# Optimization experiments

Measured on AMD Instinct MI355X. Metric: run time of the kernel, lower is better.

Reference implementation:

```python
import jax, jax.numpy as jnp
import numpy as np

B, L, D, H, DH, DFF, NL, A = 32, 1024, 512, 8, 64, 2048, 6, 21
CL = 4  # new variables per clique (chain junction tree)


def _build_mask():
    # Mirrors _make_junction_tree_mask: each position attends to itself,
    # to all parent-clique variables, and to earlier vars in its own clique.
    m = np.zeros((L, L), dtype=bool)
    for c in range(L // CL):
        own = range(c * CL, (c + 1) * CL)
        par = range((c - 1) * CL, c * CL) if c > 0 else range(0)
        for i in own:
            m[i, i] = True
            for p in par:
                m[i, p] = True
            for v in own:
                if v < i:
                    m[i, v] = True
    return m


def setup_inputs() -> dict:
    key = jax.random.key(0)
    ks = jax.random.split(key, 12)
    s = 0.02
    inp = {
        "x": jax.random.randint(ks[0], (B, L), 0, A, dtype=jnp.int32),
        "mask": jnp.asarray(_build_mask())[None, None],  # (1,1,L,L), broadcasts over B,H
        "tok_emb": jax.random.normal(ks[1], (A, D)) * s,
        "pos_emb": jax.random.normal(ks[2], (L, D)) * s,
        "wq": jax.random.normal(ks[3], (NL, D, D)) * s,
        "bq": jnp.zeros((NL, D)),
        "wk": jax.random.normal(ks[4], (NL, D, D)) * s,
        "bk": jnp.zeros((NL, D)),
        "wv": jax.random.normal(ks[5], (NL, D, D)) * s,
        "bv": jnp.zeros((NL, D)),
        "wo": jax.random.normal(ks[6], (NL, D, D)) * s,
        "bo": jnp.zeros((NL, D)),
        "ln1_s": jnp.ones((NL, D)),
        "ln1_b": jnp.zeros((NL, D)),
        "ln2_s": jnp.ones((NL, D)),
        "ln2_b": jnp.zeros((NL, D)),
        "w1": jax.random.normal(ks[7], (NL, D, DFF)) * s,
        "b1": jnp.zeros((NL, DFF)),
        "w2": jax.random.normal(ks[8], (NL, DFF, D)) * s,
        "b2": jnp.zeros((NL, D)),
        "wout": jax.random.normal(ks[9], (D, A)) * s,
        "bout": jnp.zeros((A,)),
    }
    return inp


def _ln(x, s, b):
    mu = x.mean(-1, keepdims=True)
    var = ((x - mu) ** 2).mean(-1, keepdims=True)
    return (x - mu) * jax.lax.rsqrt(var + 1e-6) * s + b


def reference(x, mask, tok_emb, pos_emb, wq, bq, wk, bk, wv, bv, wo, bo,
              ln1_s, ln1_b, ln2_s, ln2_b, w1, b1, w2, b2, wout, bout):
    h = tok_emb[x] + pos_emb[None, :, :]           # (B, L, D)
    neg = jnp.asarray(-1e9, h.dtype)
    scale = jnp.asarray(1.0 / np.sqrt(DH), h.dtype)
    for l in range(NL):
        # masked multi-head self-attention (pre-LN block)
        hn = _ln(h, ln1_s[l], ln1_b[l])
        q = (hn @ wq[l] + bq[l]).reshape(B, L, H, DH)
        k = (hn @ wk[l] + bk[l]).reshape(B, L, H, DH)
        v = (hn @ wv[l] + bv[l]).reshape(B, L, H, DH)
        sc = jnp.einsum('blhd,bmhd->bhlm', q, k) * scale
        sc = jnp.where(mask, sc, neg)              # junction-tree sparsity pattern
        attn = jax.nn.softmax(sc, axis=-1)
        o = jnp.einsum('bhlm,bmhd->blhd', attn, v).reshape(B, L, D) @ wo[l] + bo[l]
        h = h + o
        # feed-forward
        hn = _ln(h, ln2_s[l], ln2_b[l])
        h = h + (jax.nn.gelu(hn @ w1[l] + b1[l]) @ w2[l] + b2[l])
    return h @ wout + bout                          # (B, L, alphabet_size)
```

## Files before the change

### kernel.cpp

```cpp
#include <hip/hip_runtime.h>

#define BB 32
#define LL 1024
#define DD 512
#define HH 8
#define DHH 64
#define DFF 2048
#define NLAYERS 6
#define AA 21
#define MTOT (BB*LL)
#define QS 1536

typedef unsigned short u16;
typedef __bf16 bf16x8 __attribute__((ext_vector_type(8)));
typedef float f32x4 __attribute__((ext_vector_type(4)));
typedef u16 u16x8 __attribute__((ext_vector_type(8)));

__device__ __forceinline__ float bf2f(u16 u) {
    return __uint_as_float(((unsigned int)u) << 16);
}
__device__ __forceinline__ u16 f2bf(float f) {
    unsigned int i = __float_as_uint(f);
    unsigned int r = i + 0x7FFFu + ((i >> 16) & 1u);
    return (u16)(r >> 16);
}

__global__ void detect_kernel(const void* __restrict__ tok, int* __restrict__ flag) {
    __shared__ int cnt[256];
    int t = threadIdx.x;
    const u16* p = (const u16*)tok;
    int c = 0;
    #pragma unroll
    for (int j = 0; j < 8; j++) {
        u16 u = p[2 * (t * 8 + j)];
        int e = (u >> 7) & 0xFF;
        c += (e >= 97 && e <= 137) ? 1 : 0;
    }
    cnt[t] = c;
    __syncthreads();
    for (int s = 128; s; s >>= 1) {
        if (t < s) cnt[t] += cnt[t + s];
        __syncthreads();
    }
    if (t == 0) flag[0] = (cnt[0] > 1024) ? 1 : 0;
}

#define NTAB 13
struct ConvTab {
    const void* src[NTAB];
    unsigned long long dstOff[NTAB];
    int n[NTAB];
    int chunk[NTAB];
    int lstride[NTAB];
};
__global__ __launch_bounds__(256) void conv_small(ConvTab tab, u16* __restrict__ spBase,
                                                  const int* __restrict__ flag, int total) {
    int i = blockIdx.x * 256 + threadIdx.x;
    if (i >= total) return;
    int fl = flag[0];
    #pragma unroll 1
    for (int e = 0; e < NTAB; e++) {
        if (i < tab.n[e]) {
            const void* s = tab.src[e];
            u16 val = fl ? ((const u16*)s)[i] : f2bf(((const float*)s)[i]);
            int c = i / tab.chunk[e];
            int r = i - c * tab.chunk[e];
            spBase[tab.dstOff[e] + (size_t)c * tab.lstride[e] + r] = val;
            return;
        }
        i -= tab.n[e];
    }
}

__global__ __launch_bounds__(256) void conv_T(const void* __restrict__ src,
                                              u16* __restrict__ dst, int R, int C,
                                              const int* __restrict__ flag, int dstZS) {
    __shared__ u16 tile[32][33];
    int z = blockIdx.z;
    size_t zoffS = (size_t)z * R * C;
    size_t zoffD = (size_t)z * dstZS;
    int bx = blockIdx.x * 32, by = blockIdx.y * 32;
    int tx = threadIdx.x & 31, ty = threadIdx.x >> 5;
    int fl = flag[0];
    const u16* s16 = (const u16*)src + zoffS;
    const float* s32 = (const float*)src + zoffS;
    #pragma unroll
    for (int r = 0; r < 4; r++) {
        size_t idx = (size_t)(by + ty * 4 + r) * C + bx + tx;
        tile[ty * 4 + r][tx] = fl ? s16[idx] : f2bf(s32[idx]);
    }
    __syncthreads();
    #pragma unroll
    for (int r = 0; r < 4; r++)
        dst[zoffD + (size_t)(bx + ty * 4 + r) * R + by + tx] = tile[tx][ty * 4 + r];
}

__global__ __launch_bounds__(256) void woutpad_kernel(const void* __restrict__ wout,
                                                      const void* __restrict__ bout,
                                                      u16* __restrict__ wpad,
                                                      u16* __restrict__ bpad,
                                                      const int* __restrict__ flag) {
    int i = blockIdx.x * 256 + threadIdx.x;
    int fl = flag[0];
    if (i < 128 * 512) {
        int n = i >> 9, kk = i & 511;
        u16 val = 0;
        if (n < AA) val = fl ? ((const u16*)wout)[kk * AA + n] : f2bf(((const float*)wout)[kk * AA + n]);
        wpad[(size_t)n * 512 + kk] = val;
    }
    if (i < 128) {
        u16 val = 0;
        if (i < AA) val = fl ? ((const u16*)bout)[i] : f2bf(((const float*)bout)[i]);
        bpad[i] = val;
    }
}

__global__ __launch_bounds__(128) void embed_kernel(const int* __restrict__ x,
                                                    const u16* __restrict__ tok_emb,
                                                    const u16* __restrict__ pos_emb,
                                                    float* __restrict__ h) {
    int row = blockIdx.x;
    int l = row & (LL - 1);
    int tok = x[row];
    int c = threadIdx.x * 4;
    ushort4 te = *(const ushort4*)(tok_emb + (size_t)tok * DD + c);
    ushort4 pe = *(const ushort4*)(pos_emb + (size_t)l * DD + c);
    float4 o;
    o.x = bf2f(te.x) + bf2f(pe.x);
    o.y = bf2f(te.y) + bf2f(pe.y);
    o.z = bf2f(te.z) + bf2f(pe.z);
    o.w = bf2f(te.w) + bf2f(pe.w);
    *(float4*)(h + (size_t)row * DD + c) = o;
}

__global__ __launch_bounds__(256) void ln_kernel(const float* __restrict__ h,
                                                 const u16* __restrict__ s,
                                                 const u16* __restrict__ b,
                                                 u16* __restrict__ outp) {
    int row = blockIdx.x * 4 + (threadIdx.x >> 6);
    int lane = threadIdx.x & 63;
    const float* hr = h + (size_t)row * DD + lane * 8;
    f32x4 v0 = *(const f32x4*)hr;
    f32x4 v1 = *(const f32x4*)(hr + 4);
    float sum = v0[0]+v0[1]+v0[2]+v0[3]+v1[0]+v1[1]+v1[2]+v1[3];
    #pragma unroll
    for (int off = 32; off; off >>= 1) sum += __shfl_xor(sum, off, 64);
    float mu = sum * (1.0f / DD);
    float var = 0.f;
    #pragma unroll
    for (int i = 0; i < 4; i++) {
        float d0 = v0[i] - mu, d1 = v1[i] - mu;
        var += d0 * d0 + d1 * d1;
    }
    #pragma unroll
    for (int off = 32; off; off >>= 1) var += __shfl_xor(var, off, 64);
    float rs = rsqrtf(var * (1.0f / DD) + 1e-6f);
    u16x8 sv = *(const u16x8*)(s + lane * 8);
    u16x8 bv = *(const u16x8*)(b + lane * 8);
    u16x8 o;
    #pragma unroll
    for (int i = 0; i < 8; i++) {
        float xv = (i < 4) ? v0[i] : v1[i - 4];
        o[i] = f2bf((xv - mu) * rs * bf2f(sv[i]) + bf2f(bv[i]));
    }
    *(u16x8*)(outp + (size_t)row * DD + lane * 8) = o;
}

#define GLD16(gp, lp) __builtin_amdgcn_global_load_lds( \
    (const __attribute__((address_space(1))) void*)(gp), \
    (__attribute__((address_space(3))) void*)(lp), 16, 0, 0)
#define WAIT_VM(n) asm volatile("s_waitcnt vmcnt(" #n ") lgkmcnt(0)" ::: "memory")

template <int EPI>
__global__ __launch_bounds__(256) void gemm_bt(const u16* __restrict__ A,
                                               const u16* __restrict__ BT,
                                               const u16* __restrict__ bias,
                                               u16* __restrict__ Cb,
                                               float* __restrict__ Cf,
                                               int M, int N, int K, int lda,
                                               const int* __restrict__ flag) {
    __shared__ __align__(16) u16 Als[3][128 * 32];
    __shared__ __align__(16) u16 Bls[3][128 * 32];
    const int tid  = threadIdx.x;
    const int lane = tid & 63;
    const int wave = tid >> 6;

    int gx = gridDim.x, gy = gridDim.y;
    int tileX, tileY;
    if ((gy & 7) == 0) {
        int bid = blockIdx.y * gx + blockIdx.x;
        int xcd = bid & 7;
        int idx = bid >> 3;
        int stripe = gy >> 3;
        tileX = idx % gx;
        tileY = xcd * stripe + idx / gx;
    } else {
        tileX = blockIdx.x; tileY = blockIdx.y;
    }
    const int tileM = tileY * 128;
    const int tileN = tileX * 128;
    const int wm = (wave & 1) * 64;
    const int wn = (wave >> 1) * 64;

    const int srow = tid >> 2;
    const int scol = (((tid & 3) ^ ((tid >> 3) & 3))) * 8;

    const u16* Ag0 = A  + (size_t)(tileM + srow) * lda + scol;
    const u16* Ag1 = A  + (size_t)(tileM + 64 + srow) * lda + scol;
    const u16* Bg0 = BT + (size_t)(tileN + srow) * K + scol;
    const u16* Bg1 = BT + (size_t)(tileN + 64 + srow) * K + scol;

    f32x4 acc[4][4] = {};
    const int lm = lane & 15;
    const int lk = (((lane >> 4) ^ ((lm >> 1) & 3))) * 8;

    const int nk = K >> 5;

    {
        GLD16(Ag0, Als[0] + tid * 8);
        GLD16(Ag1, Als[0] + 2048 + tid * 8);
        GLD16(Bg0, Bls[0] + tid * 8);
        GLD16(Bg1, Bls[0] + 2048 + tid * 8);
        GLD16(Ag0 + 32, Als[1] + tid * 8);
        GLD16(Ag1 + 32, Als[1] + 2048 + tid * 8);
        GLD16(Bg0 + 32, Bls[1] + tid * 8);
        GLD16(Bg1 + 32, Bls[1] + 2048 + tid * 8);
    }
    WAIT_VM(4);
    __builtin_amdgcn_s_barrier();

    int cur = 0;
    int stg = 2;
    for (int kt = 0; kt < nk; kt++) {
        if (kt + 2 < nk) {
            const int k2 = (kt + 2) << 5;
            GLD16(Ag0 + k2, Als[stg] + tid * 8);
            GLD16(Ag1 + k2, Als[stg] + 2048 + tid * 8);
            GLD16(Bg0 + k2, Bls[stg] + tid * 8);
            GLD16(Bg1 + k2, Bls[stg] + 2048 + tid * 8);
        }
        bf16x8 af[4], bfr[4];
        #pragma unroll
        for (int i = 0; i < 4; i++)
            af[i] = *(const bf16x8*)(Als[cur] + (wm + i * 16 + lm) * 32 + lk);
        #pragma unroll
        for (int j = 0; j < 4; j++)
            bfr[j] = *(const bf16x8*)(Bls[cur] + (wn + j * 16 + lm) * 32 + lk);
        #pragma unroll
        for (int i = 0; i < 4; i++)
            #pragma unroll
            for (int j = 0; j < 4; j++)
                acc[i][j] = __builtin_amdgcn_mfma_f32_16x16x32_bf16(af[i], bfr[j], acc[i][j], 0, 0, 0);
        if (kt + 1 < nk) {
            if (kt + 2 < nk) WAIT_VM(4);
            else             WAIT_VM(0);
            __builtin_amdgcn_s_barrier();
        }
        cur = (cur == 2) ? 0 : cur + 1;
        stg = (stg == 2) ? 0 : stg + 1;
    }

    int fl = 0;
    if constexpr (EPI == 3) fl = flag[0];
    const int r0 = (lane >> 4) * 4;
    #pragma unroll
    for (int j = 0; j < 4; j++) {
        int col = tileN + wn + j * 16 + lm;
        float bv = bf2f(bias[col]);
        #pragma unroll
        for (int i = 0; i < 4; i++) {
            int row = tileM + wm + i * 16 + r0;
            #pragma unroll
            for (int r = 0; r < 4; r++) {
                float xv = acc[i][j][r] + bv;
                if constexpr (EPI == 0) {
                    Cb[(size_t)(row + r) * N + col] = f2bf(xv);
                } else if constexpr (EPI == 1) {
                    float u = 1.5957691216057308f * (xv + 0.044715f * xv * xv * xv);
                    float t = 1.0f - 2.0f / (__expf(u) + 1.0f);
                    Cb[(size_t)(row + r) * N + col] = f2bf(0.5f * xv * (1.0f + t));
                } else if constexpr (EPI == 2) {
                    Cf[(size_t)(row + r) * N + col] += xv;
                } else if constexpr (EPI == 4) {
                    size_t idx = (size_t)(row + r) * N + col;
                    Cb[idx] = f2bf(xv + Cf[idx]);
                } else {
                    if (col < AA) {
                        size_t idx = (size_t)(row + r) * AA + col;
                        if (fl) Cb[idx] = f2bf(xv);
                        else    Cf[idx] = xv;
                    }
                }
            }
        }
    }
}

__global__ __launch_bounds__(256) void attn_kernel(u16* qkv) {
    int bl   = blockIdx.x * 4 + (threadIdx.x >> 6);
    int lane = threadIdx.x & 63;
    int l    = bl & (LL - 1);
    int lo   = (l & ~3) - 4; if (lo < 0) lo = 0;
    int nj   = l - lo + 1;

    size_t qrow = (size_t)bl * QS;
    int off = lane * 8;

    u16x8 q8 = *(const u16x8*)(qkv + qrow + off);
    float qf[8];
    #pragma unroll
    for (int i = 0; i < 8; i++) qf[i] = bf2f(q8[i]) * 0.125f;

    size_t base = (size_t)(bl - (l - lo)) * QS;
    float sc[8];
    u16x8 v8[8];
    #pragma unroll
    for (int j = 0; j < 8; j++) {
        int jc = (j < nj) ? j : (nj - 1);
        const u16* krow = qkv + base + (size_t)jc * QS;
        u16x8 k8 = *(const u16x8*)(krow + 512 + off);
        v8[j]    = *(const u16x8*)(krow + 1024 + off);
        float t = 0.f;
        #pragma unroll
        for (int i = 0; i < 8; i++) t = fmaf(qf[i], bf2f(k8[i]), t);
        t += __shfl_xor(t, 1, 64);
        t += __shfl_xor(t, 2, 64);
        t += __shfl_xor(t, 4, 64);
        sc[j] = (j < nj) ? t : -1e30f;
    }
    float m = sc[0];
    #pragma unroll
    for (int j = 1; j < 8; j++) m = fmaxf(m, sc[j]);
    float p[8], den = 0.f;
    #pragma unroll
    for (int j = 0; j < 8; j++) { p[j] = __expf(sc[j] - m); den += p[j]; }
    float inv = 1.0f / den;
    float o[8] = {};
    #pragma unroll
    for (int j = 0; j < 8; j++)
        #pragma unroll
        for (int i = 0; i < 8; i++) o[i] = fmaf(p[j], bf2f(v8[j][i]), o[i]);
    u16x8 ov;
    #pragma unroll
    for (int i = 0; i < 8; i++) ov[i] = f2bf(o[i] * inv);
    *(u16x8*)(qkv + qrow + off) = ov;
}

extern "C" void kernel_launch(void* const* d_in, const int* in_sizes, int n_in,
                              void* d_out, int out_size, void* d_ws, size_t ws_size,
                              hipStream_t stream) {
    const int base = n_in - 22;
    const int*  x    = (const int*)d_in[0];
    const void* tokI = d_in[2 + base];
    const void* posI = d_in[3 + base];
    const void* wqI  = d_in[4 + base];
    const void* bqI  = d_in[5 + base];
    const void* wkI  = d_in[6 + base];
    const void* bkI  = d_in[7 + base];
    const void* wvI  = d_in[8 + base];
    const void* bvI  = d_in[9 + base];
    const void* woI  = d_in[10 + base];
    const void* boI  = d_in[11 + base];
    const void* ln1sI = d_in[12 + base];
    const void* ln1bI = d_in[13 + base];
    const void* ln2sI = d_in[14 + base];
    const void* ln2bI = d_in[15 + base];
    const void* w1I  = d_in[16 + base];
    const void* b1I  = d_in[17 + base];
    const void* w2I  = d_in[18 + base];
    const void* b2I  = d_in[19 + base];
    const void* woutI = d_in[20 + base];
    const void* boutI = d_in[21 + base];

    char* ws = (char*)d_ws;
    float* h   = (float*)(ws + 0);
    u16*  hn   = (u16*)(ws + 67108864);
    u16*  qkv  = (u16*)(ws + 100663296);
    u16*  wT   = (u16*)(ws + 201326592);
    u16*  sp   = (u16*)(ws + 239075328);
    int* flag  = (int*)(ws + 240500736);

    u16* mid = qkv;

    u16* wqkvT = wT;
    u16* woT   = wT + 4718592;
    u16* w1T   = wT + 6291456;
    u16* w2T   = wT + 12582912;

    const unsigned long long oWoutPad = 0;
    const unsigned long long oBoutPad = 65536;
    const unsigned long long oTok     = 65664;
    const unsigned long long oPos     = 76416;
    const unsigned long long oQkvB    = 600704;
    const unsigned long long oBo      = 609920;
    const unsigned long long oB1      = 612992;
    const unsigned long long oB2      = 625280;
    const unsigned long long oLn1s    = 628352;
    const unsigned long long oLn1b    = 631424;
    const unsigned long long oLn2s    = 634496;
    const unsigned long long oLn2b    = 637568;

    detect_kernel<<<1, 256, 0, stream>>>(tokI, flag);

    ConvTab tab;
    const void* srcs[NTAB] = {tokI, bqI, bkI, bvI, boI, b1I, b2I, ln1sI, ln1bI, ln2sI, ln2bI, posI, tokI};
    unsigned long long offs[NTAB] = {oTok, oQkvB, oQkvB + 512, oQkvB + 1024, oBo, oB1, oB2,
                                     oLn1s, oLn1b, oLn2s, oLn2b, oPos, oTok};
    int ns[NTAB]     = {10752, 3072, 3072, 3072, 3072, 12288, 3072, 3072, 3072, 3072, 3072, 524288, 0};
    int chunks[NTAB] = {10752, 512, 512, 512, 3072, 12288, 3072, 3072, 3072, 3072, 3072, 524288, 1};
    int lstr[NTAB]   = {10752, 1536, 1536, 1536, 3072, 12288, 3072, 3072, 3072, 3072, 3072, 524288, 1};
    int total = 0;
    for (int e = 0; e < NTAB; e++) {
        tab.src[e] = srcs[e]; tab.dstOff[e] = offs[e]; tab.n[e] = ns[e];
        tab.chunk[e] = chunks[e]; tab.lstride[e] = lstr[e];
        total += ns[e];
    }
    conv_small<<<(total + 255) / 256, 256, 0, stream>>>(tab, sp, flag, total);
    woutpad_kernel<<<256, 256, 0, stream>>>(woutI, boutI, sp + oWoutPad, sp + oBoutPad, flag);

    conv_T<<<dim3(16, 16, 6), 256, 0, stream>>>(wqI, wqkvT,          DD, DD, flag, 786432);
    conv_T<<<dim3(16, 16, 6), 256, 0, stream>>>(wkI, wqkvT + 262144, DD, DD, flag, 786432);
    conv_T<<<dim3(16, 16, 6), 256, 0, stream>>>(wvI, wqkvT + 524288, DD, DD, flag, 786432);
    conv_T<<<dim3(16, 16, 6), 256, 0, stream>>>(woI, woT, DD, DD, flag, 262144);
    conv_T<<<dim3(64, 16, 6), 256, 0, stream>>>(w1I, w1T, DD, DFF, flag, 1048576);
    conv_T<<<dim3(16, 64, 6), 256, 0, stream>>>(w2I, w2T, DFF, DD, flag, 1048576);

    embed_kernel<<<MTOT, 128, 0, stream>>>(x, sp + oTok, sp + oPos, h);

    for (int l = 0; l < NLAYERS; l++) {
        u16* wqkvTl = wqkvT + (size_t)l * 786432;
        u16* woTl   = woT + (size_t)l * 262144;
        u16* w1Tl   = w1T + (size_t)l * 1048576;
        u16* w2Tl   = w2T + (size_t)l * 1048576;

        ln_kernel<<<MTOT / 4, 256, 0, stream>>>(h, sp + oLn1s + l * DD, sp + oLn1b + l * DD, hn);

        gemm_bt<0><<<dim3(QS / 128, MTOT / 128), 256, 0, stream>>>(
            hn, wqkvTl, sp + oQkvB + l * QS, qkv, nullptr, MTOT, QS, DD, DD, flag);

        attn_kernel<<<MTOT / 4, 256, 0, stream>>>(qkv);

        gemm_bt<2><<<dim3(DD / 128, MTOT / 128), 256, 0, stream>>>(
            qkv, woTl, sp + oBo + l * DD, nullptr, h, MTOT, DD, DD, QS, flag);

        ln_kernel<<<MTOT / 4, 256, 0, stream>>>(h, sp + oLn2s + l * DD, sp + oLn2b + l * DD, hn);

        for (int half = 0; half < 2; half++) {
            const u16* Ahn = hn + (size_t)half * 16384 * DD;
            float* hHalf = h + (size_t)half * 16384 * DD;
            gemm_bt<1><<<dim3(DFF / 128, 16384 / 128), 256, 0, stream>>>(
                Ahn, w1Tl, sp + oB1 + l * DFF, mid, nullptr, 16384, DFF, DD, DD, flag);
            if (l < NLAYERS - 1) {
                gemm_bt<2><<<dim3(DD / 128, 16384 / 128), 256, 0, stream>>>(
                    mid, w2Tl, sp + oB2 + l * DD, nullptr, hHalf, 16384, DD, DFF, DFF, flag);
            } else {
                gemm_bt<4><<<dim3(DD / 128, 16384 / 128), 256, 0, stream>>>(
                    mid, w2Tl, sp + oB2 + l * DD, hn + (size_t)half * 16384 * DD, hHalf,
                    16384, DD, DFF, DFF, flag);
            }
        }
    }

    gemm_bt<3><<<dim3(1, MTOT / 128), 256, 0, stream>>>(
        hn, sp + oWoutPad, sp + oBoutPad, (u16*)d_out, (float*)d_out, MTOT, 128, DD, DD, flag);
}
```

Measured before the change: 2.833 ms.

## Add 256x256 eight-wave GEMM with phased load/MFMA interleave for layer matmuls

Adds a new GEMM kernel with 512 threads, 256-wide N tiles and 256- or 128-row M tiles, BK=64 double-buffered LDS and an XOR swizzle. Each k-step is split into four phases that interleave global-to-LDS staging of the next tile with MFMA work, using barriers and raised wave priority. XCD-aware tile remapping is kept. All transformer-layer GEMMs (QKV, output projection, FFN up and down) now use it, aiming for more operand reuse per load and better latency hiding. Larger tiles use more LDS and registers, which may lower occupancy and leaves fewer blocks for the smaller GEMMs.

```diff
diff --git a/kernel.cpp b/kernel.cpp
--- a/kernel.cpp
+++ b/kernel.cpp
@@ -215,7 +215,6 @@
     const int lk = (((lane >> 4) ^ ((lm >> 1) & 3))) * 8;
 
     const int nk = K >> 5;
-
     {
         GLD16(Ag0, Als[0] + tid * 8);
         GLD16(Ag1, Als[0] + 2048 + tid * 8);
@@ -229,8 +228,7 @@
     WAIT_VM(4);
     __builtin_amdgcn_s_barrier();
 
-    int cur = 0;
-    int stg = 2;
+    int cur = 0, stg = 2;
     for (int kt = 0; kt < nk; kt++) {
         if (kt + 2 < nk) {
             const int k2 = (kt + 2) << 5;
@@ -296,6 +294,155 @@
     }
 }
 
+template <int EPI, int MREP>
+__global__ __launch_bounds__(512, 2) void gemm8p(const u16* __restrict__ A,
+                                                 const u16* __restrict__ BT,
+                                                 const u16* __restrict__ bias,
+                                                 u16* __restrict__ Cb,
+                                                 float* __restrict__ Cf,
+                                                 int M, int N, int K, int lda,
+                                                 const int* __restrict__ flag) {
+    constexpr int BM  = MREP * 32;
+    constexpr int ASW = BM / 64;
+    constexpr int FI  = MREP / 2;
+    __shared__ __align__(16) u16 Als[2][BM * 64];
+    __shared__ __align__(16) u16 Bls[2][256 * 64];
+
+    const int tid  = threadIdx.x;
+    const int lane = tid & 63;
+    const int wave = tid >> 6;
+    const int wm = wave & 1;
+    const int wn = wave >> 1;
+
+    int gx = gridDim.x, gy = gridDim.y;
+    int tileX, tileY;
+    if ((gy & 7) == 0) {
+        int bid = blockIdx.y * gx + blockIdx.x;
+        int xcd = bid & 7;
+        int idx = bid >> 3;
+        int stripe = gy >> 3;
+        tileX = idx % gx;
+        tileY = xcd * stripe + idx / gx;
+    } else {
+        tileX = blockIdx.x; tileY = blockIdx.y;
+    }
+    const int tileM = tileY * BM;
+    const int tileN = tileX * 256;
+
+    const int grow = tid >> 3;
+    const int gcol = ((tid & 7) ^ (grow & 7)) * 8;
+    const u16* Ag = A  + (size_t)(tileM + grow) * lda + gcol;
+    const u16* Bg = BT + (size_t)(tileN + grow) * K + gcol;
+
+#define STAGE_A(ktn, s) GLD16(Ag + (size_t)((s) * 64) * lda + (ktn) * 64, \
+                              Als[(ktn) & 1] + (s) * 4096 + tid * 8)
+#define STAGE_B(ktn, s) GLD16(Bg + (size_t)((s) * 64) * K + (ktn) * 64, \
+                              Bls[(ktn) & 1] + (s) * 4096 + tid * 8)
+
+    f32x4 acc[MREP][4] = {};
+    const int lm = lane & 15;
+    const int kg = lane >> 4;
+    const int sw0 = ((kg)     ^ (lm & 7)) * 8;
+    const int sw1 = ((4 + kg) ^ (lm & 7)) * 8;
+    const int nk = K >> 6;
+
+#define PHASE8(curb, mh, nh, ...) do {                                              \
+    const u16* Ab_ = Als[curb];                                                     \
+    const u16* Bb_ = Bls[curb];                                                     \
+    bf16x8 af_[FI][2], bf_[2][2];                                                   \
+    _Pragma("unroll")                                                               \
+    for (int i = 0; i < FI; i++) {                                                  \
+        int arow = wm * (MREP * 16) + (mh) * (MREP * 8) + i * 16 + lm;              \
+        af_[i][0] = *(const bf16x8*)(Ab_ + arow * 64 + sw0);                        \
+        af_[i][1] = *(const bf16x8*)(Ab_ + arow * 64 + sw1);                        \
+    }                                                                               \
+    _Pragma("unroll")                                                               \
+    for (int j = 0; j < 2; j++) {                                                   \
+        int brow = wn * 64 + (nh) * 32 + j * 16 + lm;                               \
+        bf_[j][0] = *(const bf16x8*)(Bb_ + brow * 64 + sw0);                        \
+        bf_[j][1] = *(const bf16x8*)(Bb_ + brow * 64 + sw1);                        \
+    }                                                                               \
+    __VA_ARGS__                                                                     \
+    __builtin_amdgcn_s_barrier();                                                   \
+    __builtin_amdgcn_s_setprio(1);                                                  \
+    _Pragma("unroll")                                                               \
+    for (int ks = 0; ks < 2; ks++)                                                  \
+        _Pragma("unroll")                                                           \
+        for (int i = 0; i < FI; i++)                                                \
+            _Pragma("unroll")                                                       \
+            for (int j = 0; j < 2; j++)                                             \
+                acc[(mh) * FI + i][(nh) * 2 + j] =                                  \
+                    __builtin_amdgcn_mfma_f32_16x16x32_bf16(                        \
+                        af_[i][ks], bf_[j][ks], acc[(mh) * FI + i][(nh) * 2 + j],   \
+                        0, 0, 0);                                                   \
+    __builtin_amdgcn_s_setprio(0);                                                  \
+} while (0)
+
+    #pragma unroll
+    for (int s = 0; s < ASW; s++) STAGE_A(0, s);
+    #pragma unroll
+    for (int s = 0; s < 4; s++)  STAGE_B(0, s);
+    WAIT_VM(0);
+    __builtin_amdgcn_s_barrier();
+
+    #pragma unroll 1
+    for (int kt = 0; kt < nk; kt++) {
+        const int cur = kt & 1;
+        const int ktn = kt + 1;
+        const bool st = ktn < nk;
+        if constexpr (MREP == 8) {
+            PHASE8(cur, 0, 0, if (st) { STAGE_A(ktn, 0); STAGE_A(ktn, 1); STAGE_B(ktn, 0); });
+            __builtin_amdgcn_s_barrier();
+            PHASE8(cur, 1, 0, if (st) { STAGE_A(ktn, 2); STAGE_A(ktn, 3); STAGE_B(ktn, 1); });
+            __builtin_amdgcn_s_barrier();
+            PHASE8(cur, 0, 1, if (st) { STAGE_B(ktn, 2); STAGE_B(ktn, 3); });
+            __builtin_amdgcn_s_barrier();
+            PHASE8(cur, 1, 1, {});
+        } else {
+            PHASE8(cur, 0, 0, if (st) { STAGE_A(ktn, 0); STAGE_B(ktn, 0); });
+            __builtin_amdgcn_s_barrier();
+            PHASE8(cur, 1, 0, if (st) { STAGE_A(ktn, 1); STAGE_B(ktn, 1); });
+            __builtin_amdgcn_s_barrier();
+            PHASE8(cur, 0, 1, if (st) { STAGE_B(ktn, 2); STAGE_B(ktn, 3); });
+            __builtin_amdgcn_s_barrier();
+            PHASE8(cur, 1, 1, {});
+        }
+        WAIT_VM(0);
+        __builtin_amdgcn_s_barrier();
+    }
+
+    (void)flag;
+    const int r0 = (lane >> 4) * 4;
+    #pragma unroll
+    for (int j = 0; j < 4; j++) {
+        int col = tileN + wn * 64 + j * 16 + lm;
+        float bvf = bf2f(bias[col]);
+        #pragma unroll
+        for (int i = 0; i < MREP; i++) {
+            int row = tileM + wm * (MREP * 16) + i * 16 + r0;
+            #pragma unroll
+            for (int r = 0; r < 4; r++) {
+                float xv = acc[i][j][r] + bvf;
+                if constexpr (EPI == 0) {
+                    Cb[(size_t)(row + r) * N + col] = f2bf(xv);
+                } else if constexpr (EPI == 1) {
+                    float u = 1.5957691216057308f * (xv + 0.044715f * xv * xv * xv);
+                    float t = 1.0f - 2.0f / (__expf(u) + 1.0f);
+                    Cb[(size_t)(row + r) * N + col] = f2bf(0.5f * xv * (1.0f + t));
+                } else if constexpr (EPI == 2) {
+                    Cf[(size_t)(row + r) * N + col] += xv;
+                } else if constexpr (EPI == 4) {
+                    size_t idx = (size_t)(row + r) * N + col;
+                    Cb[idx] = f2bf(xv + Cf[idx]);
+                }
+            }
+        }
+    }
+#undef PHASE8
+#undef STAGE_A
+#undef STAGE_B
+}
+
 __global__ __launch_bounds__(256) void attn_kernel(u16* qkv) {
     int bl   = blockIdx.x * 4 + (threadIdx.x >> 6);
     int lane = threadIdx.x & 63;
@@ -435,12 +582,12 @@
 
         ln_kernel<<<MTOT / 4, 256, 0, stream>>>(h, sp + oLn1s + l * DD, sp + oLn1b + l * DD, hn);
 
-        gemm_bt<0><<<dim3(QS / 128, MTOT / 128), 256, 0, stream>>>(
+        gemm8p<0, 8><<<dim3(QS / 256, MTOT / 256), 512, 0, stream>>>(
             hn, wqkvTl, sp + oQkvB + l * QS, qkv, nullptr, MTOT, QS, DD, DD, flag);
 
         attn_kernel<<<MTOT / 4, 256, 0, stream>>>(qkv);
 
-        gemm_bt<2><<<dim3(DD / 128, MTOT / 128), 256, 0, stream>>>(
+        gemm8p<2, 8><<<dim3(DD / 256, MTOT / 256), 512, 0, stream>>>(
             qkv, woTl, sp + oBo + l * DD, nullptr, h, MTOT, DD, DD, QS, flag);
 
         ln_kernel<<<MTOT / 4, 256, 0, stream>>>(h, sp + oLn2s + l * DD, sp + oLn2b + l * DD, hn);
@@ -448,13 +595,13 @@
         for (int half = 0; half < 2; half++) {
             const u16* Ahn = hn + (size_t)half * 16384 * DD;
             float* hHalf = h + (size_t)half * 16384 * DD;
-            gemm_bt<1><<<dim3(DFF / 128, 16384 / 128), 256, 0, stream>>>(
+            gemm8p<1, 8><<<dim3(DFF / 256, 16384 / 256), 512, 0, stream>>>(
                 Ahn, w1Tl, sp + oB1 + l * DFF, mid, nullptr, 16384, DFF, DD, DD, flag);
             if (l < NLAYERS - 1) {
-                gemm_bt<2><<<dim3(DD / 128, 16384 / 128), 256, 0, stream>>>(
+                gemm8p<2, 4><<<dim3(DD / 256, 16384 / 128), 512, 0, stream>>>(
                     mid, w2Tl, sp + oB2 + l * DD, nullptr, hHalf, 16384, DD, DFF, DFF, flag);
             } else {
-                gemm_bt<4><<<dim3(DD / 128, 16384 / 128), 256, 0, stream>>>(
+                gemm8p<4, 4><<<dim3(DD / 256, 16384 / 128), 512, 0, stream>>>(
                     mid, w2Tl, sp + oB2 + l * DD, hn + (size_t)half * 16384 * DD, hHalf,
                     16384, DD, DFF, DFF, flag);
             }
```

After: 2.841 ms. About the same (+0.3%).
